# Optimization experiments

Hardware: AMD Instinct MI355X
Metric: run time of the kernel (lower is better)

## Reference

```python
import jax, jax.numpy as jnp
import numpy as np

N_IN = 28 * 28   # flattened MNIST image
H1 = 100         # layer1 hidden size (hardcoded in module)
H2 = 10          # layer2 hidden size (hardcoded in module)
DECAY = 0.9
THRESH = 1.0
PEN = 1.5
T = 100          # n_time_steps
BEGIN = 20       # begin_eval
BATCH = 4096


def setup_inputs() -> dict:
    key = jax.random.key(0)
    k1, k2, kx = jax.random.split(key, 3)
    # xavier_uniform init as in init_parameters()
    lim1 = float(np.sqrt(6.0 / (N_IN + H1)))
    lim2 = float(np.sqrt(6.0 / (H1 + H2)))
    W1 = jax.random.uniform(k1, (N_IN, H1), jnp.float32, -lim1, lim1)
    b1 = jnp.zeros((H1,), jnp.float32)
    W2 = jax.random.uniform(k2, (H1, H2), jnp.float32, -lim2, lim2)
    b2 = jnp.zeros((H2,), jnp.float32)
    x = jax.random.uniform(kx, (BATCH, 1, 28, 28), jnp.float32)
    return {"x": x, "W1": W1, "b1": b1, "W2": W2, "b2": b2}


def _neuron_step(prev_inner, prev_outer, x, W, b):
    # leaky-integrate-and-fire update; returns new state plus the DELAYED
    # (previous-step) state/output, as in SpikingNeuronLayerRNN.forward
    input_excitation = x @ W + b
    inner = input_excitation + prev_inner * DECAY
    outer = jax.nn.relu(inner - THRESH)
    gate = (outer > 0).astype(inner.dtype)          # non-differentiable gate
    inner = inner - gate * (PEN / THRESH * inner)   # penalty reset
    return inner, outer, prev_inner, prev_outer


def reference(x, W1, b1, W2, b2):
    B = x.shape[0]
    xf = x.reshape(B, -1)                           # [B, 784]
    z1 = jnp.zeros((B, H1), xf.dtype)
    z2 = jnp.zeros((B, H2), xf.dtype)

    def step(carry, key):
        pi1, po1, pi2, po2 = carry
        # InputDataToSpikingPerceptronLayer: random gating of the image
        xi = jax.random.uniform(key, xf.shape, xf.dtype) * xf
        ni1, no1, d_state1, d_out1 = _neuron_step(pi1, po1, xi, W1, b1)
        ni2, no2, d_state2, d_out2 = _neuron_step(pi2, po2, d_out1, W2, b2)
        return (ni1, no1, ni2, no2), d_state2        # collect layer2 delayed state

    keys = jax.random.split(jax.random.key(42), T)
    _, states2 = jax.lax.scan(step, (z1, z1, z2, z2), keys)  # [T, B, 10]
    # OutputDataToSpikingPerceptronLayer(average_output=False): sum over time
    out = states2[BEGIN:].sum(axis=0)                # [B, 10]
    return jax.nn.log_softmax(out, axis=-1)
```

## Files before the change

kernel.cpp:

```cpp
#include <hip/hip_runtime.h>
#include <stdint.h>
#include <math.h>

#define NIN    784
#define H1     100
#define H2     10
#define BATCH  4096
#define RT     16
#define WROWS  112
#define WK     800
#define AS     808

typedef _Float16 h16;
typedef h16  h8  __attribute__((ext_vector_type(8)));
typedef h16  h2t __attribute__((ext_vector_type(2)));
typedef float f4 __attribute__((ext_vector_type(4)));

#define L_A     0
#define L_O1S   25856
#define L_W2T   29056
#define L_RED   30056
#define L_SUMS  33640
#define L_KEYS  33800
#define L_TOTAL 34000

__device__ __forceinline__ void threefry2x32(uint32_t k0, uint32_t k1,
                                             uint32_t x0, uint32_t x1,
                                             uint32_t& o0, uint32_t& o1) {
    uint32_t ks2 = k0 ^ k1 ^ 0x1BD11BDAu;
    x0 += k0; x1 += k1;
#define TFR(r) { x0 += x1; x1 = __builtin_rotateleft32(x1, r); x1 ^= x0; }
    TFR(13) TFR(15) TFR(26) TFR(6)  x0 += k1;  x1 += ks2 + 1u;
    TFR(17) TFR(29) TFR(16) TFR(24) x0 += ks2; x1 += k0 + 2u;
    TFR(13) TFR(15) TFR(26) TFR(6)  x0 += k0;  x1 += k1 + 3u;
    TFR(17) TFR(29) TFR(16) TFR(24) x0 += k1;  x1 += ks2 + 4u;
    TFR(13) TFR(15) TFR(26) TFR(6)  x0 += ks2; x1 += k0 + 5u;
#undef TFR
    o0 = x0; o1 = x1;
}

__device__ __forceinline__ float u01(uint32_t b) {
    return __uint_as_float((b >> 9) | 0x3f800000u) - 1.0f;
}

__global__ void prep_w1(const float* __restrict__ W1, h16* __restrict__ w1hi,
                        h16* __restrict__ w1lo) {
    int idx = blockIdx.x * 256 + threadIdx.x;
    if (idx < WROWS * WK) {
        int h = idx / WK, k = idx - h * WK;
        float w = (h < H1 && k < NIN) ? W1[k * H1 + h] : 0.0f;
        h16 wh = (h16)w;
        h16 wl = (h16)((w - (float)wh) * 4096.0f);
        w1hi[idx] = wh; w1lo[idx] = wl;
    }
}

__global__ __launch_bounds__(1024)
void spiking_net_kernel(const float* __restrict__ x,
                        const h16* __restrict__ w1hi,
                        const h16* __restrict__ w1lo,
                        const float* __restrict__ b1,
                        const float* __restrict__ W2,
                        const float* __restrict__ b2,
                        float* __restrict__ out) {
    extern __shared__ __align__(16) float smem[];
    float*    const o1s  = smem + L_O1S;
    float*    const w2t  = smem + L_W2T;
    float*    const red  = smem + L_RED;
    float*    const sums = smem + L_SUMS;
    uint32_t* const keys = (uint32_t*)(smem + L_KEYS);

    const int tid  = threadIdx.x;
    const int wv   = tid >> 6;
    const int lane = tid & 63;
    const int row0 = blockIdx.x * RT;

    const bool mfm = (wv < 14);
    const int  nt  = wv >> 1;
    const int  kh  = wv & 1;

    if (tid < 100) {
        uint32_t y0, y1;
        threefry2x32(0u, 42u, 0u, (uint32_t)tid, y0, y1);
        keys[2 * tid] = y0; keys[2 * tid + 1] = y1;
    }
    for (int i = tid; i < H2 * H1; i += 1024) {
        int cc2 = i / H1, k = i - cc2 * H1;
        w2t[i] = W2[k * H2 + cc2];
    }
    for (int i = tid; i < 2 * RT * H1; i += 1024) o1s[i] = 0.0f;
    for (int i = tid; i < L_O1S; i += 1024) smem[i] = 0.0f;

    const int  aoff = (lane & 15) * AS + (lane >> 4) * 8;
    const int  n    = (nt << 4) + (lane & 15);
    const int  boff = n * WK + (lane >> 4) * 8;
    const bool nv   = (n < H1);
    const float b1v = (mfm && kh == 0) ? b1[nv ? n : 0] : 0.0f;
    float i1[4] = {0.f, 0.f, 0.f, 0.f};

    const int      hrow = wv;
    const uint32_t rb   = (uint32_t)((row0 + hrow) * NIN);
    const float*   xr   = x + (row0 + hrow) * NIN;

    const int  r2    = tid / 10;
    const int  c2    = tid - r2 * 10;
    const bool l2act = (tid < RT * H2);
    const float b2r  = l2act ? b2[c2] : 0.0f;
    float i2 = 0.0f, sum2 = 0.0f;

    __syncthreads();

    auto hashrow = [&](int buf, uint32_t hk0, uint32_t hk1) {
        h16* ah = (h16*)(smem + buf * 12928)        + hrow * AS;
        h16* al = (h16*)(smem + buf * 12928 + 6464) + hrow * AS;
#pragma unroll
        for (int it = 0; it < 7; ++it) {
            int kd = (it << 6) + lane;
            if (it < 6 || lane < 8) {
                uint32_t c0 = rb + (uint32_t)(2 * kd);
                uint32_t a0, a1, q0, q1;
                threefry2x32(hk0, hk1, 0u, c0,      a0, a1);
                threefry2x32(hk0, hk1, 0u, c0 + 1u, q0, q1);
                float2 xv = *(const float2*)(xr + 2 * kd);
                float v0 = u01(a0 ^ a1) * xv.x;
                float v1 = u01(q0 ^ q1) * xv.y;
                h16 hh0 = (h16)v0, hh1 = (h16)v1;
                h16 ll0 = (h16)((v0 - (float)hh0) * 4096.0f);
                h16 ll1 = (h16)((v1 - (float)hh1) * 4096.0f);
                h2t ph; ph.x = hh0; ph.y = hh1;
                h2t pl; pl.x = ll0; pl.y = ll1;
                *(h2t*)(ah + 2 * kd) = ph;
                *(h2t*)(al + 2 * kd) = pl;
            }
        }
    };

    hashrow(0, keys[0], keys[1]);
    __syncthreads();

    f4 cc;

    for (int t = 0; t < 100; ++t) {
        if (t >= 1 && t < 99 && mfm && kh == 0) {
            const float* rp = red + ((t - 1) & 1) * 1792 + nt * 256 + lane * 4;
            f4 other = *(const f4*)rp;
            float* op = o1s + ((t - 1) & 1) * 1600;
#pragma unroll
            for (int rg = 0; rg < 4; ++rg) {
                float a  = (cc[rg] + other[rg]) + b1v;
                float in = a + i1[rg] * 0.9f;
                float o  = fmaxf(in - 1.0f, 0.0f);
                in = (o > 0.0f) ? (in - 1.5f * in) : in;
                i1[rg] = in;
                if (nv) op[((lane >> 4) * 4 + rg) * H1 + n] = o;
            }
        }
        if (t < 98 && mfm) {
            const h16* Ah = (const h16*)(smem + (t & 1) * 12928);
            const h16* Al = (const h16*)(smem + (t & 1) * 12928 + 6464);
            f4 accM = {0.f, 0.f, 0.f, 0.f};
            f4 accS = {0.f, 0.f, 0.f, 0.f};
            if (kh == 0) {
#pragma unroll
                for (int kt = 0; kt < 13; ++kt) {
                    h8 avh = *(const h8*)(Ah + aoff + kt * 32);
                    h8 avl = *(const h8*)(Al + aoff + kt * 32);
                    h8 bvh = *(const h8*)(w1hi + boff + kt * 32);
                    h8 bvl = *(const h8*)(w1lo + boff + kt * 32);
                    accM = __builtin_amdgcn_mfma_f32_16x16x32_f16(avh, bvh, accM, 0, 0, 0);
                    accS = __builtin_amdgcn_mfma_f32_16x16x32_f16(avl, bvh, accS, 0, 0, 0);
                    accS = __builtin_amdgcn_mfma_f32_16x16x32_f16(avh, bvl, accS, 0, 0, 0);
                }
            } else {
#pragma unroll
                for (int kt = 13; kt < 25; ++kt) {
                    h8 avh = *(const h8*)(Ah + aoff + kt * 32);
                    h8 avl = *(const h8*)(Al + aoff + kt * 32);
                    h8 bvh = *(const h8*)(w1hi + boff + kt * 32);
                    h8 bvl = *(const h8*)(w1lo + boff + kt * 32);
                    accM = __builtin_amdgcn_mfma_f32_16x16x32_f16(avh, bvh, accM, 0, 0, 0);
                    accS = __builtin_amdgcn_mfma_f32_16x16x32_f16(avl, bvh, accS, 0, 0, 0);
                    accS = __builtin_amdgcn_mfma_f32_16x16x32_f16(avh, bvl, accS, 0, 0, 0);
                }
            }
            cc = accM + accS * 0.000244140625f;
            if (kh == 1) *(f4*)(red + (t & 1) * 1792 + nt * 256 + lane * 4) = cc;
        }
        if (t < 97) hashrow((t + 1) & 1, keys[2 * (t + 1)], keys[2 * (t + 1) + 1]);
        if (t >= 1 && l2act) {
            const float* orow = o1s + (t & 1) * 1600 + r2 * H1;
            const float* wrow = &w2t[c2 * H1];
            float a = 0.0f;
#pragma unroll
            for (int k = 0; k < H1; k += 4) {
                float4 ov = *(const float4*)&orow[k];
                float4 wq = *(const float4*)&wrow[k];
                a = fmaf(ov.x, wq.x, a); a = fmaf(ov.y, wq.y, a);
                a = fmaf(ov.z, wq.z, a); a = fmaf(ov.w, wq.w, a);
            }
            float inner2 = (a + b2r) + i2 * 0.9f;
            float outer2 = fmaxf(inner2 - 1.0f, 0.0f);
            inner2 = (outer2 > 0.0f) ? (inner2 - 1.5f * inner2) : inner2;
            i2 = inner2;
            if (t >= 20) sum2 += inner2;
        }
        __syncthreads();
    }

    if (l2act) sums[r2 * H2 + c2] = sum2;
    __syncthreads();
    if (l2act) {
        float m = -INFINITY;
#pragma unroll
        for (int cc2 = 0; cc2 < H2; ++cc2) m = fmaxf(m, sums[r2 * H2 + cc2]);
        float s = 0.0f;
#pragma unroll
        for (int cc2 = 0; cc2 < H2; ++cc2) s += expf(sums[r2 * H2 + cc2] - m);
        out[(row0 + r2) * H2 + c2] = sum2 - m - logf(s);
    }
}

extern "C" void kernel_launch(void* const* d_in, const int* in_sizes, int n_in,
                              void* d_out, int out_size, void* d_ws, size_t ws_size,
                              hipStream_t stream) {
    const float* x  = (const float*)d_in[0];
    const float* W1 = (const float*)d_in[1];
    const float* b1 = (const float*)d_in[2];
    const float* W2 = (const float*)d_in[3];
    const float* b2 = (const float*)d_in[4];
    float* out = (float*)d_out;
    h16* w1hi = (h16*)d_ws;
    h16* w1lo = w1hi + WROWS * WK;

    hipLaunchKernelGGL(prep_w1, dim3((WROWS * WK + 255) / 256), dim3(256), 0, stream,
                       W1, w1hi, w1lo);

    const size_t lds_bytes = (size_t)L_TOTAL * 4;
    hipFuncSetAttribute((const void*)spiking_net_kernel,
                        hipFuncAttributeMaxDynamicSharedMemorySize, (int)lds_bytes);
    hipLaunchKernelGGL(spiking_net_kernel, dim3(BATCH / RT), dim3(1024), lds_bytes, stream,
                       x, w1hi, w1lo, b1, W2, b2, out);
}
```

Before: 1.215 ms.

## Rebalance threefry hashing across waves and move layer-2 work to spare waves

Input gating is now hashed one element per lane in flat 64-element chunks spread evenly over all 16 waves. Before, each wave hashed one row in pairs and left lanes idle on the last pass. Threefry rotates are written as v_alignbit right-rotates, and the uniform-times-x product becomes a single FMA. Layer-2 neuron updates move from the first threads onto waves 14-15, with some lanes handling two outputs, to keep them off the waves that also issue MFMAs. In exchange, the half-precision stores to LDS become scalar and each element now needs an integer divide to find its row.

```diff
diff --git a/kernel.cpp b/kernel.cpp
--- a/kernel.cpp
+++ b/kernel.cpp
@@ -13,7 +13,6 @@
 
 typedef _Float16 h16;
 typedef h16  h8  __attribute__((ext_vector_type(8)));
-typedef h16  h2t __attribute__((ext_vector_type(2)));
 typedef float f4 __attribute__((ext_vector_type(4)));
 
 #define L_A     0
@@ -24,23 +23,35 @@
 #define L_KEYS  33800
 #define L_TOTAL 34000
 
+#define RORA(x, imm) ({ uint32_t d_;                                        \
+    asm("v_alignbit_b32 %0, %1, %1, " #imm : "=v"(d_) : "v"(x)); d_; })
+
 __device__ __forceinline__ void threefry2x32(uint32_t k0, uint32_t k1,
                                              uint32_t x0, uint32_t x1,
                                              uint32_t& o0, uint32_t& o1) {
     uint32_t ks2 = k0 ^ k1 ^ 0x1BD11BDAu;
     x0 += k0; x1 += k1;
-#define TFR(r) { x0 += x1; x1 = __builtin_rotateleft32(x1, r); x1 ^= x0; }
-    TFR(13) TFR(15) TFR(26) TFR(6)  x0 += k1;  x1 += ks2 + 1u;
-    TFR(17) TFR(29) TFR(16) TFR(24) x0 += ks2; x1 += k0 + 2u;
-    TFR(13) TFR(15) TFR(26) TFR(6)  x0 += k0;  x1 += k1 + 3u;
-    TFR(17) TFR(29) TFR(16) TFR(24) x0 += k1;  x1 += ks2 + 4u;
-    TFR(13) TFR(15) TFR(26) TFR(6)  x0 += ks2; x1 += k0 + 5u;
-#undef TFR
+#define R4A { x0 += x1; x1 = RORA(x1, 19); x1 ^= x0;                        \
+              x0 += x1; x1 = RORA(x1, 17); x1 ^= x0;                        \
+              x0 += x1; x1 = RORA(x1, 6);  x1 ^= x0;                        \
+              x0 += x1; x1 = RORA(x1, 26); x1 ^= x0; }
+#define R4B { x0 += x1; x1 = RORA(x1, 15); x1 ^= x0;                        \
+              x0 += x1; x1 = RORA(x1, 3);  x1 ^= x0;                        \
+              x0 += x1; x1 = RORA(x1, 16); x1 ^= x0;                        \
+              x0 += x1; x1 = RORA(x1, 8);  x1 ^= x0; }
+    R4A x0 += k1;  x1 += ks2 + 1u;
+    R4B x0 += ks2; x1 += k0 + 2u;
+    R4A x0 += k0;  x1 += k1 + 3u;
+    R4B x0 += k1;  x1 += ks2 + 4u;
+    R4A x0 += ks2; x1 += k0 + 5u;
+#undef R4A
+#undef R4B
     o0 = x0; o1 = x1;
 }
 
-__device__ __forceinline__ float u01(uint32_t b) {
-    return __uint_as_float((b >> 9) | 0x3f800000u) - 1.0f;
+__device__ __forceinline__ float u01m(uint32_t b, float xv) {
+    float f = __uint_as_float((b >> 9) | 0x3f800000u);
+    return fmaf(f, xv, -xv);
 }
 
 __global__ void prep_w1(const float* __restrict__ W1, h16* __restrict__ w1hi,
@@ -98,52 +109,66 @@
     const float b1v = (mfm && kh == 0) ? b1[nv ? n : 0] : 0.0f;
     float i1[4] = {0.f, 0.f, 0.f, 0.f};
 
-    const int      hrow = wv;
-    const uint32_t rb   = (uint32_t)((row0 + hrow) * NIN);
-    const float*   xr   = x + (row0 + hrow) * NIN;
-
-    const int  r2    = tid / 10;
-    const int  c2    = tid - r2 * 10;
-    const bool l2act = (tid < RT * H2);
-    const float b2r  = l2act ? b2[c2] : 0.0f;
-    float i2 = 0.0f, sum2 = 0.0f;
+    const int hcnt  = (wv >= 10 && wv < 14) ? 13 : 12;
+    const int hbase = 12 * wv + ((wv >= 10) ? ((wv < 14) ? (wv - 10) : 4) : 0);
+    const uint32_t rb0 = (uint32_t)(row0 * NIN);
+    const float* xb = x + row0 * NIN;
+
+    const bool l2a = (wv >= 14);
+    const int  u   = l2a ? ((wv - 14) * 64 + lane) : 0;
+    const bool l2b = l2a && (u >= 48 && u < 80);
+    const int  pa  = u;
+    const int  pb  = l2b ? (128 + u - 48) : 0;
+    const int  r2a = pa / 10, c2a = pa - 10 * r2a;
+    const int  r2b = pb / 10, c2b = pb - 10 * r2b;
+    const float b2a = l2a ? b2[c2a] : 0.0f;
+    const float b2b = l2b ? b2[c2b] : 0.0f;
+    float i2a = 0.f, s2a = 0.f, i2b = 0.f, s2b = 0.f;
 
     __syncthreads();
 
-    auto hashrow = [&](int buf, uint32_t hk0, uint32_t hk1) {
-        h16* ah = (h16*)(smem + buf * 12928)        + hrow * AS;
-        h16* al = (h16*)(smem + buf * 12928 + 6464) + hrow * AS;
-#pragma unroll
-        for (int it = 0; it < 7; ++it) {
-            int kd = (it << 6) + lane;
-            if (it < 6 || lane < 8) {
-                uint32_t c0 = rb + (uint32_t)(2 * kd);
-                uint32_t a0, a1, q0, q1;
-                threefry2x32(hk0, hk1, 0u, c0,      a0, a1);
-                threefry2x32(hk0, hk1, 0u, c0 + 1u, q0, q1);
-                float2 xv = *(const float2*)(xr + 2 * kd);
-                float v0 = u01(a0 ^ a1) * xv.x;
-                float v1 = u01(q0 ^ q1) * xv.y;
-                h16 hh0 = (h16)v0, hh1 = (h16)v1;
-                h16 ll0 = (h16)((v0 - (float)hh0) * 4096.0f);
-                h16 ll1 = (h16)((v1 - (float)hh1) * 4096.0f);
-                h2t ph; ph.x = hh0; ph.y = hh1;
-                h2t pl; pl.x = ll0; pl.y = ll1;
-                *(h2t*)(ah + 2 * kd) = ph;
-                *(h2t*)(al + 2 * kd) = pl;
-            }
-        }
+    auto do_hash = [&](int buf, int ch, uint32_t hk0, uint32_t hk1) {
+        int e = (ch << 6) + lane;
+        uint32_t y0, y1;
+        threefry2x32(hk0, hk1, 0u, rb0 + (uint32_t)e, y0, y1);
+        float v = u01m(y0 ^ y1, xb[e]);
+        h16 hh = (h16)v;
+        h16 ll = (h16)((v - (float)hh) * 4096.0f);
+        int r = e / NIN, j = e - r * NIN;
+        h16* ah = (h16*)(smem + buf * 12928) + r * AS + j;
+        ah[0] = hh;
+        ah[12928] = ll;
     };
-
-    hashrow(0, keys[0], keys[1]);
+    auto hash_step = [&](int buf, uint32_t hk0, uint32_t hk1) {
+#pragma unroll 2
+        for (int ci = 0; ci < hcnt; ++ci) do_hash(buf, hbase + ci, hk0, hk1);
+    };
+    auto layer2 = [&](const float* orow, float wb2, float& i2, float& s2,
+                      int c2, bool dosum) {
+        const float* wrow = &w2t[c2 * H1];
+        float a = 0.0f;
+#pragma unroll
+        for (int k = 0; k < H1; k += 4) {
+            float4 ov = *(const float4*)&orow[k];
+            float4 wq = *(const float4*)&wrow[k];
+            a = fmaf(ov.x, wq.x, a); a = fmaf(ov.y, wq.y, a);
+            a = fmaf(ov.z, wq.z, a); a = fmaf(ov.w, wq.w, a);
+        }
+        float inner2 = (a + wb2) + i2 * 0.9f;
+        float outer2 = fmaxf(inner2 - 1.0f, 0.0f);
+        inner2 = (outer2 > 0.0f) ? (inner2 - 1.5f * inner2) : inner2;
+        i2 = inner2;
+        if (dosum) s2 += inner2;
+    };
+
+    hash_step(0, keys[0], keys[1]);
     __syncthreads();
 
     f4 cc;
 
     for (int t = 0; t < 100; ++t) {
         if (t >= 1 && t < 99 && mfm && kh == 0) {
-            const float* rp = red + ((t - 1) & 1) * 1792 + nt * 256 + lane * 4;
-            f4 other = *(const f4*)rp;
+            f4 other = *(const f4*)(red + ((t - 1) & 1) * 1792 + nt * 256 + lane * 4);
             float* op = o1s + ((t - 1) & 1) * 1600;
 #pragma unroll
             for (int rg = 0; rg < 4; ++rg) {
@@ -157,7 +182,7 @@
         }
         if (t < 98 && mfm) {
             const h16* Ah = (const h16*)(smem + (t & 1) * 12928);
-            const h16* Al = (const h16*)(smem + (t & 1) * 12928 + 6464);
+            const h16* Al = Ah + 12928;
             f4 accM = {0.f, 0.f, 0.f, 0.f};
             f4 accS = {0.f, 0.f, 0.f, 0.f};
             if (kh == 0) {
@@ -186,37 +211,26 @@
             cc = accM + accS * 0.000244140625f;
             if (kh == 1) *(f4*)(red + (t & 1) * 1792 + nt * 256 + lane * 4) = cc;
         }
-        if (t < 97) hashrow((t + 1) & 1, keys[2 * (t + 1)], keys[2 * (t + 1) + 1]);
-        if (t >= 1 && l2act) {
-            const float* orow = o1s + (t & 1) * 1600 + r2 * H1;
-            const float* wrow = &w2t[c2 * H1];
-            float a = 0.0f;
-#pragma unroll
-            for (int k = 0; k < H1; k += 4) {
-                float4 ov = *(const float4*)&orow[k];
-                float4 wq = *(const float4*)&wrow[k];
-                a = fmaf(ov.x, wq.x, a); a = fmaf(ov.y, wq.y, a);
-                a = fmaf(ov.z, wq.z, a); a = fmaf(ov.w, wq.w, a);
-            }
-            float inner2 = (a + b2r) + i2 * 0.9f;
-            float outer2 = fmaxf(inner2 - 1.0f, 0.0f);
-            inner2 = (outer2 > 0.0f) ? (inner2 - 1.5f * inner2) : inner2;
-            i2 = inner2;
-            if (t >= 20) sum2 += inner2;
+        if (t < 97) hash_step((t + 1) & 1, keys[2 * (t + 1)], keys[2 * (t + 1) + 1]);
+        if (t >= 1 && l2a) {
+            const float* ob = o1s + (t & 1) * 1600;
+            layer2(ob + r2a * H1, b2a, i2a, s2a, c2a, t >= 20);
+            if (l2b) layer2(ob + r2b * H1, b2b, i2b, s2b, c2b, t >= 20);
         }
         __syncthreads();
     }
 
-    if (l2act) sums[r2 * H2 + c2] = sum2;
+    if (l2a) { sums[pa] = s2a; if (l2b) sums[pb] = s2b; }
     __syncthreads();
-    if (l2act) {
+    if (tid < RT * H2) {
+        const int r2 = tid / 10, c2 = tid - r2 * 10;
         float m = -INFINITY;
 #pragma unroll
         for (int cc2 = 0; cc2 < H2; ++cc2) m = fmaxf(m, sums[r2 * H2 + cc2]);
         float s = 0.0f;
 #pragma unroll
         for (int cc2 = 0; cc2 < H2; ++cc2) s += expf(sums[r2 * H2 + cc2] - m);
-        out[(row0 + r2) * H2 + c2] = sum2 - m - logf(s);
+        out[(row0 + r2) * H2 + c2] = sums[r2 * H2 + c2] - m - logf(s);
     }
 }
 
```

Result: slower. 1.458 ms (+20.0%).

## Halve rows per block to 8, split hashing across waves, dedicate layer-2 waves

Applied to the files above, without the earlier changes.

Each block now handles 8 batch rows instead of 16, so the grid has twice as many blocks and the shared-memory footprint is roughly halved, which allows more blocks per CU. Random-number hashing for each row is split between two waves, each covering half of K. The two spare waves (14 and 15) now run the layer-2 dot products, and only the first 32 lanes of each MFMA wave do the layer-1 epilogue. The MFMA path still uses 16x16 tiles with only 8 valid rows, so half of the matrix-core work is wasted, and total W1 loads from global memory double across the grid.

```diff
diff --git a/kernel.cpp b/kernel.cpp
--- a/kernel.cpp
+++ b/kernel.cpp
@@ -6,7 +6,7 @@
 #define H1     100
 #define H2     10
 #define BATCH  4096
-#define RT     16
+#define RT     8
 #define WROWS  112
 #define WK     800
 #define AS     808
@@ -17,12 +17,12 @@
 typedef float f4 __attribute__((ext_vector_type(4)));
 
 #define L_A     0
-#define L_O1S   25856
-#define L_W2T   29056
-#define L_RED   30056
-#define L_SUMS  33640
-#define L_KEYS  33800
-#define L_TOTAL 34000
+#define L_O1S   12928
+#define L_W2T   14528
+#define L_RED   15528
+#define L_SUMS  17320
+#define L_KEYS  17400
+#define L_TOTAL 17600
 
 __device__ __forceinline__ void threefry2x32(uint32_t k0, uint32_t k1,
                                              uint32_t x0, uint32_t x1,
@@ -55,7 +55,7 @@
     }
 }
 
-__global__ __launch_bounds__(1024)
+__global__ __launch_bounds__(1024, 8)
 void spiking_net_kernel(const float* __restrict__ x,
                         const h16* __restrict__ w1hi,
                         const h16* __restrict__ w1lo,
@@ -88,51 +88,67 @@
         int cc2 = i / H1, k = i - cc2 * H1;
         w2t[i] = W2[k * H2 + cc2];
     }
-    for (int i = tid; i < 2 * RT * H1; i += 1024) o1s[i] = 0.0f;
-    for (int i = tid; i < L_O1S; i += 1024) smem[i] = 0.0f;
-
-    const int  aoff = (lane & 15) * AS + (lane >> 4) * 8;
+    for (int i = tid; i < L_W2T; i += 1024) smem[i] = 0.0f;
+
+    const int  aoff = (lane & 7) * AS + (lane >> 4) * 8;
     const int  n    = (nt << 4) + (lane & 15);
     const int  boff = n * WK + (lane >> 4) * 8;
     const bool nv   = (n < H1);
-    const float b1v = (mfm && kh == 0) ? b1[nv ? n : 0] : 0.0f;
+    const bool live = (lane < 32);
+    const float b1v = (mfm && kh == 0 && live) ? b1[nv ? n : 0] : 0.0f;
     float i1[4] = {0.f, 0.f, 0.f, 0.f};
 
-    const int      hrow = wv;
-    const uint32_t rb   = (uint32_t)((row0 + hrow) * NIN);
-    const float*   xr   = x + (row0 + hrow) * NIN;
-
-    const int  r2    = tid / 10;
-    const int  c2    = tid - r2 * 10;
-    const bool l2act = (tid < RT * H2);
-    const float b2r  = l2act ? b2[c2] : 0.0f;
-    float i2 = 0.0f, sum2 = 0.0f;
+    const int      hr  = wv & 7;
+    const int      hf  = wv >> 3;
+    const int      hkb = hf ? 192 : 0;
+    const uint32_t rb  = (uint32_t)((row0 + hr) * NIN);
+    const float*   xr  = x + (row0 + hr) * NIN;
+
+    const bool l2w = (wv >= 14);
+    const int  u   = l2w ? ((wv - 14) * 64 + lane) : 0;
+    const bool l2a = l2w && (u < RT * H2);
+    const int  r2  = u / 10, c2 = u - 10 * r2;
+    const float b2r = l2a ? b2[c2] : 0.0f;
+    float i2 = 0.f, sum2 = 0.f;
 
     __syncthreads();
 
+    auto do_kd = [&](h16* ah, int kd, uint32_t hk0, uint32_t hk1) {
+        uint32_t c0 = rb + (uint32_t)(2 * kd);
+        uint32_t a0, a1, q0, q1;
+        threefry2x32(hk0, hk1, 0u, c0,      a0, a1);
+        threefry2x32(hk0, hk1, 0u, c0 + 1u, q0, q1);
+        float2 xv = *(const float2*)(xr + 2 * kd);
+        float v0 = u01(a0 ^ a1) * xv.x;
+        float v1 = u01(q0 ^ q1) * xv.y;
+        h16 hh0 = (h16)v0, hh1 = (h16)v1;
+        h16 ll0 = (h16)((v0 - (float)hh0) * 4096.0f);
+        h16 ll1 = (h16)((v1 - (float)hh1) * 4096.0f);
+        h2t ph; ph.x = hh0; ph.y = hh1;
+        h2t pl; pl.x = ll0; pl.y = ll1;
+        *(h2t*)(ah + 2 * kd) = ph;
+        *(h2t*)(ah + 6464 + 2 * kd) = pl;
+    };
     auto hashrow = [&](int buf, uint32_t hk0, uint32_t hk1) {
-        h16* ah = (h16*)(smem + buf * 12928)        + hrow * AS;
-        h16* al = (h16*)(smem + buf * 12928 + 6464) + hrow * AS;
-#pragma unroll
-        for (int it = 0; it < 7; ++it) {
-            int kd = (it << 6) + lane;
-            if (it < 6 || lane < 8) {
-                uint32_t c0 = rb + (uint32_t)(2 * kd);
-                uint32_t a0, a1, q0, q1;
-                threefry2x32(hk0, hk1, 0u, c0,      a0, a1);
-                threefry2x32(hk0, hk1, 0u, c0 + 1u, q0, q1);
-                float2 xv = *(const float2*)(xr + 2 * kd);
-                float v0 = u01(a0 ^ a1) * xv.x;
-                float v1 = u01(q0 ^ q1) * xv.y;
-                h16 hh0 = (h16)v0, hh1 = (h16)v1;
-                h16 ll0 = (h16)((v0 - (float)hh0) * 4096.0f);
-                h16 ll1 = (h16)((v1 - (float)hh1) * 4096.0f);
-                h2t ph; ph.x = hh0; ph.y = hh1;
-                h2t pl; pl.x = ll0; pl.y = ll1;
-                *(h2t*)(ah + 2 * kd) = ph;
-                *(h2t*)(al + 2 * kd) = pl;
-            }
-        }
+        h16* ah = (h16*)smem + buf * 12928 + hr * AS;
+#pragma unroll
+        for (int it = 0; it < 3; ++it) do_kd(ah, hkb + (it << 6) + lane, hk0, hk1);
+        if (hf && lane < 8) do_kd(ah, hkb + 192 + lane, hk0, hk1);
+    };
+    auto layer2 = [&](const float* orow) {
+        const float* wrow = &w2t[c2 * H1];
+        float a = 0.0f;
+#pragma unroll
+        for (int k = 0; k < H1; k += 4) {
+            float4 ov = *(const float4*)&orow[k];
+            float4 wq = *(const float4*)&wrow[k];
+            a = fmaf(ov.x, wq.x, a); a = fmaf(ov.y, wq.y, a);
+            a = fmaf(ov.z, wq.z, a); a = fmaf(ov.w, wq.w, a);
+        }
+        float inner2 = (a + b2r) + i2 * 0.9f;
+        float outer2 = fmaxf(inner2 - 1.0f, 0.0f);
+        inner2 = (outer2 > 0.0f) ? (inner2 - 1.5f * inner2) : inner2;
+        i2 = inner2;
     };
 
     hashrow(0, keys[0], keys[1]);
@@ -141,10 +157,9 @@
     f4 cc;
 
     for (int t = 0; t < 100; ++t) {
-        if (t >= 1 && t < 99 && mfm && kh == 0) {
-            const float* rp = red + ((t - 1) & 1) * 1792 + nt * 256 + lane * 4;
-            f4 other = *(const f4*)rp;
-            float* op = o1s + ((t - 1) & 1) * 1600;
+        if (t >= 1 && t < 99 && mfm && kh == 0 && live) {
+            f4 other = *(const f4*)(red + ((t - 1) & 1) * 896 + nt * 128 + lane * 4);
+            float* op = o1s + ((t - 1) & 1) * 800;
 #pragma unroll
             for (int rg = 0; rg < 4; ++rg) {
                 float a  = (cc[rg] + other[rg]) + b1v;
@@ -156,8 +171,8 @@
             }
         }
         if (t < 98 && mfm) {
-            const h16* Ah = (const h16*)(smem + (t & 1) * 12928);
-            const h16* Al = (const h16*)(smem + (t & 1) * 12928 + 6464);
+            const h16* Ah = (const h16*)smem + (t & 1) * 12928;
+            const h16* Al = Ah + 6464;
             f4 accM = {0.f, 0.f, 0.f, 0.f};
             f4 accS = {0.f, 0.f, 0.f, 0.f};
             if (kh == 0) {
@@ -184,39 +199,28 @@
                 }
             }
             cc = accM + accS * 0.000244140625f;
-            if (kh == 1) *(f4*)(red + (t & 1) * 1792 + nt * 256 + lane * 4) = cc;
+            if (kh == 1 && live)
+                *(f4*)(red + (t & 1) * 896 + nt * 128 + lane * 4) = cc;
         }
         if (t < 97) hashrow((t + 1) & 1, keys[2 * (t + 1)], keys[2 * (t + 1) + 1]);
-        if (t >= 1 && l2act) {
-            const float* orow = o1s + (t & 1) * 1600 + r2 * H1;
-            const float* wrow = &w2t[c2 * H1];
-            float a = 0.0f;
-#pragma unroll
-            for (int k = 0; k < H1; k += 4) {
-                float4 ov = *(const float4*)&orow[k];
-                float4 wq = *(const float4*)&wrow[k];
-                a = fmaf(ov.x, wq.x, a); a = fmaf(ov.y, wq.y, a);
-                a = fmaf(ov.z, wq.z, a); a = fmaf(ov.w, wq.w, a);
-            }
-            float inner2 = (a + b2r) + i2 * 0.9f;
-            float outer2 = fmaxf(inner2 - 1.0f, 0.0f);
-            inner2 = (outer2 > 0.0f) ? (inner2 - 1.5f * inner2) : inner2;
-            i2 = inner2;
-            if (t >= 20) sum2 += inner2;
+        if (t >= 1 && l2a) {
+            layer2(o1s + (t & 1) * 800 + r2 * H1);
+            if (t >= 20) sum2 += i2;
         }
         __syncthreads();
     }
 
-    if (l2act) sums[r2 * H2 + c2] = sum2;
+    if (l2a) sums[u] = sum2;
     __syncthreads();
-    if (l2act) {
+    if (tid < RT * H2) {
+        const int rr = tid / 10, ccl = tid - 10 * rr;
         float m = -INFINITY;
 #pragma unroll
-        for (int cc2 = 0; cc2 < H2; ++cc2) m = fmaxf(m, sums[r2 * H2 + cc2]);
+        for (int cc2 = 0; cc2 < H2; ++cc2) m = fmaxf(m, sums[rr * H2 + cc2]);
         float s = 0.0f;
 #pragma unroll
-        for (int cc2 = 0; cc2 < H2; ++cc2) s += expf(sums[r2 * H2 + cc2] - m);
-        out[(row0 + r2) * H2 + c2] = sum2 - m - logf(s);
+        for (int cc2 = 0; cc2 < H2; ++cc2) s += expf(sums[rr * H2 + cc2] - m);
+        out[(row0 + rr) * H2 + ccl] = sums[rr * H2 + ccl] - m - logf(s);
     }
 }
 
```

Result: slower. 1.691 ms (+39.1%).

## Interleave next-step hashing with MFMA loop and move layer2 to idle waves

Applied to the files above, without the earlier changes.

The threefry hashing of the next time step's input row is now interleaved inside the MFMA k-loop on the matrix waves, so ALU hashing work can overlap with matrix instructions instead of running after them. Layer-2 dot products move off the first 160 threads onto the two non-MFMA waves (14 and 15), with some lanes handling two outputs. This spreads per-step work more evenly across waves to shorten the per-iteration critical path before the barrier. It adds register pressure in the MFMA loop and changes the lo-plane address to a fixed offset from the hi plane.

```diff
diff --git a/kernel.cpp b/kernel.cpp
--- a/kernel.cpp
+++ b/kernel.cpp
@@ -102,121 +102,150 @@
     const uint32_t rb   = (uint32_t)((row0 + hrow) * NIN);
     const float*   xr   = x + (row0 + hrow) * NIN;
 
-    const int  r2    = tid / 10;
-    const int  c2    = tid - r2 * 10;
-    const bool l2act = (tid < RT * H2);
-    const float b2r  = l2act ? b2[c2] : 0.0f;
-    float i2 = 0.0f, sum2 = 0.0f;
+    const bool l2w = (wv >= 14);
+    const int  u   = l2w ? ((wv - 14) * 64 + lane) : 0;
+    const bool l2b = l2w && (u >= 48 && u < 80);
+    const int  pa  = u;
+    const int  pb  = l2b ? (128 + u - 48) : 0;
+    const int  r2a = pa / 10, c2a = pa - 10 * r2a;
+    const int  r2b = pb / 10, c2b = pb - 10 * r2b;
+    const float b2a = l2w ? b2[c2a] : 0.0f;
+    const float b2b = l2b ? b2[c2b] : 0.0f;
+    float i2a = 0.f, s2a = 0.f, i2b = 0.f, s2b = 0.f;
 
     __syncthreads();
 
-    auto hashrow = [&](int buf, uint32_t hk0, uint32_t hk1) {
-        h16* ah = (h16*)(smem + buf * 12928)        + hrow * AS;
-        h16* al = (h16*)(smem + buf * 12928 + 6464) + hrow * AS;
-#pragma unroll
-        for (int it = 0; it < 7; ++it) {
-            int kd = (it << 6) + lane;
-            if (it < 6 || lane < 8) {
-                uint32_t c0 = rb + (uint32_t)(2 * kd);
-                uint32_t a0, a1, q0, q1;
-                threefry2x32(hk0, hk1, 0u, c0,      a0, a1);
-                threefry2x32(hk0, hk1, 0u, c0 + 1u, q0, q1);
-                float2 xv = *(const float2*)(xr + 2 * kd);
-                float v0 = u01(a0 ^ a1) * xv.x;
-                float v1 = u01(q0 ^ q1) * xv.y;
-                h16 hh0 = (h16)v0, hh1 = (h16)v1;
-                h16 ll0 = (h16)((v0 - (float)hh0) * 4096.0f);
-                h16 ll1 = (h16)((v1 - (float)hh1) * 4096.0f);
-                h2t ph; ph.x = hh0; ph.y = hh1;
-                h2t pl; pl.x = ll0; pl.y = ll1;
-                *(h2t*)(ah + 2 * kd) = ph;
-                *(h2t*)(al + 2 * kd) = pl;
-            }
+    auto do_kd = [&](h16* ah, int it, uint32_t hk0, uint32_t hk1) {
+        int kd = (it << 6) + lane;
+        if (it < 6 || lane < 8) {
+            uint32_t c0 = rb + (uint32_t)(2 * kd);
+            uint32_t a0, a1, q0, q1;
+            threefry2x32(hk0, hk1, 0u, c0,      a0, a1);
+            threefry2x32(hk0, hk1, 0u, c0 + 1u, q0, q1);
+            float2 xv = *(const float2*)(xr + 2 * kd);
+            float v0 = u01(a0 ^ a1) * xv.x;
+            float v1 = u01(q0 ^ q1) * xv.y;
+            h16 hh0 = (h16)v0, hh1 = (h16)v1;
+            h16 ll0 = (h16)((v0 - (float)hh0) * 4096.0f);
+            h16 ll1 = (h16)((v1 - (float)hh1) * 4096.0f);
+            h2t ph; ph.x = hh0; ph.y = hh1;
+            h2t pl; pl.x = ll0; pl.y = ll1;
+            *(h2t*)(ah + 2 * kd) = ph;
+            *(h2t*)(ah + 12928 + 2 * kd) = pl;
         }
     };
-
-    hashrow(0, keys[0], keys[1]);
+    auto layer2 = [&](const float* orow, float wb2, float& i2, float& s2,
+                      int c2, bool dosum) {
+        const float* wrow = &w2t[c2 * H1];
+        float a = 0.0f;
+#pragma unroll
+        for (int k = 0; k < H1; k += 4) {
+            float4 ov = *(const float4*)&orow[k];
+            float4 wq = *(const float4*)&wrow[k];
+            a = fmaf(ov.x, wq.x, a); a = fmaf(ov.y, wq.y, a);
+            a = fmaf(ov.z, wq.z, a); a = fmaf(ov.w, wq.w, a);
+        }
+        float inner2 = (a + wb2) + i2 * 0.9f;
+        float outer2 = fmaxf(inner2 - 1.0f, 0.0f);
+        inner2 = (outer2 > 0.0f) ? (inner2 - 1.5f * inner2) : inner2;
+        i2 = inner2;
+        if (dosum) s2 += inner2;
+    };
+
+    {
+        h16* ah = (h16*)(smem + 0) + hrow * AS;
+#pragma unroll
+        for (int it = 0; it < 7; ++it) do_kd(ah, it, keys[0], keys[1]);
+    }
     __syncthreads();
 
     f4 cc;
 
     for (int t = 0; t < 100; ++t) {
-        if (t >= 1 && t < 99 && mfm && kh == 0) {
-            const float* rp = red + ((t - 1) & 1) * 1792 + nt * 256 + lane * 4;
-            f4 other = *(const f4*)rp;
-            float* op = o1s + ((t - 1) & 1) * 1600;
-#pragma unroll
-            for (int rg = 0; rg < 4; ++rg) {
-                float a  = (cc[rg] + other[rg]) + b1v;
-                float in = a + i1[rg] * 0.9f;
-                float o  = fmaxf(in - 1.0f, 0.0f);
-                in = (o > 0.0f) ? (in - 1.5f * in) : in;
-                i1[rg] = in;
-                if (nv) op[((lane >> 4) * 4 + rg) * H1 + n] = o;
-            }
-        }
-        if (t < 98 && mfm) {
+        const bool domf = (t < 98);
+        const bool doh  = (t < 97);
+        const uint32_t hk0 = keys[2 * (t + 1)], hk1 = keys[2 * (t + 1) + 1];
+
+        if (mfm) {
+            if (t >= 1 && t < 99 && kh == 0) {
+                f4 other = *(const f4*)(red + ((t - 1) & 1) * 1792 + nt * 256 + lane * 4);
+                float* op = o1s + ((t - 1) & 1) * 1600;
+#pragma unroll
+                for (int rg = 0; rg < 4; ++rg) {
+                    float a  = (cc[rg] + other[rg]) + b1v;
+                    float in = a + i1[rg] * 0.9f;
+                    float o  = fmaxf(in - 1.0f, 0.0f);
+                    in = (o > 0.0f) ? (in - 1.5f * in) : in;
+                    i1[rg] = in;
+                    if (nv) op[((lane >> 4) * 4 + rg) * H1 + n] = o;
+                }
+            }
             const h16* Ah = (const h16*)(smem + (t & 1) * 12928);
-            const h16* Al = (const h16*)(smem + (t & 1) * 12928 + 6464);
+            const h16* Al = Ah + 12928;
+            h16* hw = (h16*)(smem + ((t + 1) & 1) * 12928) + hrow * AS;
             f4 accM = {0.f, 0.f, 0.f, 0.f};
             f4 accS = {0.f, 0.f, 0.f, 0.f};
             if (kh == 0) {
 #pragma unroll
-                for (int kt = 0; kt < 13; ++kt) {
-                    h8 avh = *(const h8*)(Ah + aoff + kt * 32);
-                    h8 avl = *(const h8*)(Al + aoff + kt * 32);
-                    h8 bvh = *(const h8*)(w1hi + boff + kt * 32);
-                    h8 bvl = *(const h8*)(w1lo + boff + kt * 32);
-                    accM = __builtin_amdgcn_mfma_f32_16x16x32_f16(avh, bvh, accM, 0, 0, 0);
-                    accS = __builtin_amdgcn_mfma_f32_16x16x32_f16(avl, bvh, accS, 0, 0, 0);
-                    accS = __builtin_amdgcn_mfma_f32_16x16x32_f16(avh, bvl, accS, 0, 0, 0);
+                for (int j = 0; j < 13; ++j) {
+                    if (doh && j < 7) do_kd(hw, j, hk0, hk1);
+                    if (domf) {
+                        const int kt = j;
+                        h8 avh = *(const h8*)(Ah + aoff + kt * 32);
+                        h8 avl = *(const h8*)(Al + aoff + kt * 32);
+                        h8 bvh = *(const h8*)(w1hi + boff + kt * 32);
+                        h8 bvl = *(const h8*)(w1lo + boff + kt * 32);
+                        accM = __builtin_amdgcn_mfma_f32_16x16x32_f16(avh, bvh, accM, 0, 0, 0);
+                        accS = __builtin_amdgcn_mfma_f32_16x16x32_f16(avl, bvh, accS, 0, 0, 0);
+                        accS = __builtin_amdgcn_mfma_f32_16x16x32_f16(avh, bvl, accS, 0, 0, 0);
+                    }
                 }
             } else {
 #pragma unroll
-                for (int kt = 13; kt < 25; ++kt) {
-                    h8 avh = *(const h8*)(Ah + aoff + kt * 32);
-                    h8 avl = *(const h8*)(Al + aoff + kt * 32);
-                    h8 bvh = *(const h8*)(w1hi + boff + kt * 32);
-                    h8 bvl = *(const h8*)(w1lo + boff + kt * 32);
-                    accM = __builtin_amdgcn_mfma_f32_16x16x32_f16(avh, bvh, accM, 0, 0, 0);
-                    accS = __builtin_amdgcn_mfma_f32_16x16x32_f16(avl, bvh, accS, 0, 0, 0);
-                    accS = __builtin_amdgcn_mfma_f32_16x16x32_f16(avh, bvl, accS, 0, 0, 0);
+                for (int j = 0; j < 12; ++j) {
+                    if (doh && j < 7) do_kd(hw, j, hk0, hk1);
+                    if (domf) {
+                        const int kt = 13 + j;
+                        h8 avh = *(const h8*)(Ah + aoff + kt * 32);
+                        h8 avl = *(const h8*)(Al + aoff + kt * 32);
+                        h8 bvh = *(const h8*)(w1hi + boff + kt * 32);
+                        h8 bvl = *(const h8*)(w1lo + boff + kt * 32);
+                        accM = __builtin_amdgcn_mfma_f32_16x16x32_f16(avh, bvh, accM, 0, 0, 0);
+                        accS = __builtin_amdgcn_mfma_f32_16x16x32_f16(avl, bvh, accS, 0, 0, 0);
+                        accS = __builtin_amdgcn_mfma_f32_16x16x32_f16(avh, bvl, accS, 0, 0, 0);
+                    }
                 }
             }
-            cc = accM + accS * 0.000244140625f;
-            if (kh == 1) *(f4*)(red + (t & 1) * 1792 + nt * 256 + lane * 4) = cc;
-        }
-        if (t < 97) hashrow((t + 1) & 1, keys[2 * (t + 1)], keys[2 * (t + 1) + 1]);
-        if (t >= 1 && l2act) {
-            const float* orow = o1s + (t & 1) * 1600 + r2 * H1;
-            const float* wrow = &w2t[c2 * H1];
-            float a = 0.0f;
-#pragma unroll
-            for (int k = 0; k < H1; k += 4) {
-                float4 ov = *(const float4*)&orow[k];
-                float4 wq = *(const float4*)&wrow[k];
-                a = fmaf(ov.x, wq.x, a); a = fmaf(ov.y, wq.y, a);
-                a = fmaf(ov.z, wq.z, a); a = fmaf(ov.w, wq.w, a);
-            }
-            float inner2 = (a + b2r) + i2 * 0.9f;
-            float outer2 = fmaxf(inner2 - 1.0f, 0.0f);
-            inner2 = (outer2 > 0.0f) ? (inner2 - 1.5f * inner2) : inner2;
-            i2 = inner2;
-            if (t >= 20) sum2 += inner2;
+            if (domf) {
+                cc = accM + accS * 0.000244140625f;
+                if (kh == 1) *(f4*)(red + (t & 1) * 1792 + nt * 256 + lane * 4) = cc;
+            }
+        } else {
+            if (doh) {
+                h16* hw = (h16*)(smem + ((t + 1) & 1) * 12928) + hrow * AS;
+#pragma unroll
+                for (int it = 0; it < 7; ++it) do_kd(hw, it, hk0, hk1);
+            }
+            if (t >= 1) {
+                const float* ob = o1s + (t & 1) * 1600;
+                layer2(ob + r2a * H1, b2a, i2a, s2a, c2a, t >= 20);
+                if (l2b) layer2(ob + r2b * H1, b2b, i2b, s2b, c2b, t >= 20);
+            }
         }
         __syncthreads();
     }
 
-    if (l2act) sums[r2 * H2 + c2] = sum2;
+    if (l2w) { sums[pa] = s2a; if (l2b) sums[pb] = s2b; }
     __syncthreads();
-    if (l2act) {
+    if (tid < RT * H2) {
+        const int rr = tid / 10, ccl = tid - 10 * rr;
         float m = -INFINITY;
 #pragma unroll
-        for (int cc2 = 0; cc2 < H2; ++cc2) m = fmaxf(m, sums[r2 * H2 + cc2]);
+        for (int cc2 = 0; cc2 < H2; ++cc2) m = fmaxf(m, sums[rr * H2 + cc2]);
         float s = 0.0f;
 #pragma unroll
-        for (int cc2 = 0; cc2 < H2; ++cc2) s += expf(sums[r2 * H2 + cc2] - m);
-        out[(row0 + r2) * H2 + c2] = sum2 - m - logf(s);
+        for (int cc2 = 0; cc2 < H2; ++cc2) s += expf(sums[rr * H2 + cc2] - m);
+        out[(row0 + rr) * H2 + ccl] = sums[rr * H2 + ccl] - m - logf(s);
     }
 }
 
```

Measured after the change: 1.035 ms. -14.8%, faster.
